# Optimization experiments

Measured on AMD Instinct MI355X. Metric: run time of the kernel, lower is better.

The kernel has to match this reference:

```python
import jax, jax.numpy as jnp
import numpy as np

N = 20000      # nodes
E = 200000     # edges (before self loops)
H = 8          # heads
C = 256        # out_channels per head
IN = 256       # in_channels
OUT = 250      # final linear out


def setup_inputs() -> dict:
    key = jax.random.key(0)
    ks = jax.random.split(key, 8)
    x = jax.random.normal(ks[0], (N, IN), jnp.float32)
    edge_index = jax.random.randint(ks[1], (2, E), 0, N)
    # GATConv params (lin has no bias in PyG; bias is on the conv output)
    W_gat = jax.random.normal(ks[2], (IN, H * C), jnp.float32) * 0.02
    att_src = jax.random.normal(ks[3], (H, C), jnp.float32) * 0.1
    att_dst = jax.random.normal(ks[4], (H, C), jnp.float32) * 0.1
    b_gat = jnp.zeros((H * C,), jnp.float32)
    # conv1: 1x1 conv with 1 in/out channel -> scalar weight + scalar bias
    conv_w = jax.random.normal(ks[5], (), jnp.float32)
    conv_b = jnp.zeros((), jnp.float32)
    W_lin = jax.random.normal(ks[6], (C, OUT), jnp.float32) * 0.02
    b_lin = jnp.zeros((OUT,), jnp.float32)
    return dict(x=x, edge_index=edge_index, W_gat=W_gat, att_src=att_src,
                att_dst=att_dst, b_gat=b_gat, conv_w=conv_w, conv_b=conv_b,
                W_lin=W_lin, b_lin=b_lin)


def reference(x, edge_index, W_gat, att_src, att_dst, b_gat, conv_w, conv_b, W_lin, b_lin):
    # --- GATConv (PyG defaults: add_self_loops=True, negative_slope=0.2, concat=True) ---
    loops = jnp.arange(N)
    src = jnp.concatenate([edge_index[0], loops])  # [E+N]
    dst = jnp.concatenate([edge_index[1], loops])
    xh = (x @ W_gat).reshape(N, H, C)              # [N,H,C]
    a_s = jnp.einsum('nhc,hc->nh', xh, att_src)    # [N,H]
    a_d = jnp.einsum('nhc,hc->nh', xh, att_dst)
    e = jax.nn.leaky_relu(a_s[src] + a_d[dst], 0.2)  # [E+N, H]
    # segment softmax over edges sharing a destination node
    m = jax.ops.segment_max(e, dst, num_segments=N)
    m = jnp.where(jnp.isfinite(m), m, 0.0)
    ex = jnp.exp(e - m[dst])
    s = jax.ops.segment_sum(ex, dst, num_segments=N)
    alpha = ex / (s[dst] + 1e-16)                  # [E+N, H]
    msg = xh[src] * alpha[:, :, None]              # [E+N, H, C]  (dominant traffic)
    agg = jax.ops.segment_sum(msg, dst, num_segments=N)  # [N,H,C]
    agg = agg + b_gat.reshape(H, C)
    # --- head split / pool / 1x1 conv / head softmax / fuse ---
    z = agg.transpose(1, 0, 2)                     # [H,N,C]  (torch z is [H,1,N,C])
    pooled = z.mean(axis=(1, 2))                   # [H] global avg pool
    g = jax.nn.relu(pooled * conv_w + conv_b)
    w = jax.nn.softmax(g, axis=0)                  # softmax over heads (dim=0)
    fuse = jnp.einsum('hnc,h->nc', z, w)           # sum over heads of z * w
    Hf = jax.nn.relu(fuse + x)                     # residual with input features
    return Hf @ W_lin + b_lin                      # [N, 250]
```

## Files before the change

### kernel.cpp

```cpp
#include <hip/hip_runtime.h>
#include <hip/hip_bf16.h>


typedef __attribute__((ext_vector_type(8))) short short8v;
typedef __attribute__((ext_vector_type(4))) float float4v;

__device__ __forceinline__ unsigned f2bfu(float f) {
  unsigned u = __float_as_uint(f);
  return (u + 0x7fffu + ((u >> 16) & 1u)) >> 16;
}
__device__ __forceinline__ float bfu_lo(unsigned u) { return __uint_as_float(u << 16); }
__device__ __forceinline__ float bfu_hi(unsigned u) { return __uint_as_float(u & 0xffff0000u); }
__device__ __forceinline__ unsigned pack2(float a, float b) { return f2bfu(a) | (f2bfu(b) << 16); }

__device__ __forceinline__ void ld8(const float* p, float* v) {
  float4 a = ((const float4*)p)[0], b = ((const float4*)p)[1];
  v[0] = a.x; v[1] = a.y; v[2] = a.z; v[3] = a.w;
  v[4] = b.x; v[5] = b.y; v[6] = b.z; v[7] = b.w;
}
__device__ __forceinline__ void ld4(const float* p, float* v) {
  float4 a = ((const float4*)p)[0];
  v[0] = a.x; v[1] = a.y; v[2] = a.z; v[3] = a.w;
}

__device__ __forceinline__ float bcast(float x, int e) {
  return __uint_as_float((unsigned)__builtin_amdgcn_readlane((int)__float_as_uint(x), e));
}

__device__ __forceinline__ void gll16(const void* g, void* l) {
  __builtin_amdgcn_global_load_lds(
      (__attribute__((address_space(1))) void*)const_cast<void*>(g),
      (__attribute__((address_space(3))) void*)(l), 16, 0, 0);
}

__global__ __launch_bounds__(256) void prep1_kernel(
    const float* __restrict__ W_lin, short* __restrict__ wlT,
    const float* __restrict__ W, const float* __restrict__ att_s,
    const float* __restrict__ att_d, float* __restrict__ ws_s,
    float* __restrict__ ws_d, float* __restrict__ ws_r,
    const int* __restrict__ ei, int* __restrict__ deg) {
  __shared__ float smem[4096];
  int b = blockIdx.x;
  int t = threadIdx.x;
  if (b < 64) {
    float (*tile)[33] = (float(*)[33])smem;
    int tx = t & 31, ty = t >> 5;
    int c0 = (b & 7) * 32, r0 = (b >> 3) * 32;
    #pragma unroll
    for (int j = ty; j < 32; j += 8) {
      int r = r0 + j, c = c0 + tx;
      tile[j][tx] = (c < 250) ? W_lin[(size_t)r * 250 + c] : 0.f;
    }
    __syncthreads();
    #pragma unroll
    for (int j = ty; j < 32; j += 8) {
      int c = c0 + j, r = r0 + tx;
      wlT[(size_t)c * 256 + r] = (short)f2bfu(tile[tx][j]);
    }
  } else if (b < 96) {
    float* sas = smem;
    float* sad = smem + 2048;
    for (int i = t; i < 2048; i += 256) { sas[i] = att_s[i]; sad[i] = att_d[i]; }
    __syncthreads();
    int kk = t >> 5, h = (t >> 2) & 7, q = t & 3;
    int k = (b - 64) * 8 + kk;
    const float4* wr = (const float4*)(W + (size_t)k * 2048 + h * 256 + q * 64);
    const float* as = sas + h * 256 + q * 64;
    const float* ad = sad + h * 256 + q * 64;
    float s = 0.f, dd = 0.f, r = 0.f;
    #pragma unroll
    for (int c4 = 0; c4 < 16; ++c4) {
      float4 wv = wr[c4];
      int c = c4 * 4;
      s  += wv.x * as[c] + wv.y * as[c + 1] + wv.z * as[c + 2] + wv.w * as[c + 3];
      dd += wv.x * ad[c] + wv.y * ad[c + 1] + wv.z * ad[c + 2] + wv.w * ad[c + 3];
      r  += wv.x + wv.y + wv.z + wv.w;
    }
    #pragma unroll
    for (int off = 1; off < 4; off <<= 1) {
      s += __shfl_xor(s, off);
      dd += __shfl_xor(dd, off);
      r += __shfl_xor(r, off);
    }
    if (q == 0) {
      int g = k * 8 + h;
      ws_s[g] = s;
      ws_d[g] = dd;
      ws_r[g] = r;
    }
  } else {
    int e = (b - 96) * 256 + t;
    if (e < 200000) atomicAdd(&deg[ei[200000 + e]], 1);
  }
}

__global__ __launch_bounds__(256) void asd_kernel(const float* __restrict__ x,
    const float* __restrict__ ws_s, const float* __restrict__ ws_d,
    const float* __restrict__ ws_r, float* __restrict__ a_s,
    float* __restrict__ a_d, float* __restrict__ rs, short* __restrict__ x_bf) {
  __shared__ float ls[2048], ld2[2048], lr[2048];
  int tid = threadIdx.x;
  for (int i = tid; i < 2048; i += 256) { ls[i] = ws_s[i]; ld2[i] = ws_d[i]; lr[i] = ws_r[i]; }
  __syncthreads();
  int node = blockIdx.x * 32 + (tid >> 3);
  int h = tid & 7;
  const float4* xr = (const float4*)(x + (size_t)node * 256);
  float as = 0.f, ad = 0.f, rr = 0.f;
  #pragma unroll 1
  for (int g = 0; g < 8; ++g) {
    bool own = (g == h);
    int bufi[16];
    #pragma unroll
    for (int j = 0; j < 8; ++j) {
      int k4 = g * 8 + j;
      float4 v = xr[k4];
      int k8 = k4 * 32 + h;
      as += v.x * ls[k8] + v.y * ls[k8 + 8] + v.z * ls[k8 + 16] + v.w * ls[k8 + 24];
      ad += v.x * ld2[k8] + v.y * ld2[k8 + 8] + v.z * ld2[k8 + 16] + v.w * ld2[k8 + 24];
      rr += v.x * lr[k8] + v.y * lr[k8 + 8] + v.z * lr[k8 + 16] + v.w * lr[k8 + 24];
      bufi[2 * j] = (int)pack2(v.x, v.y);
      bufi[2 * j + 1] = (int)pack2(v.z, v.w);
    }
    if (own) {
      int4* dst = (int4*)(x_bf + (size_t)node * 256 + h * 32);
      dst[0] = make_int4(bufi[0], bufi[1], bufi[2], bufi[3]);
      dst[1] = make_int4(bufi[4], bufi[5], bufi[6], bufi[7]);
      dst[2] = make_int4(bufi[8], bufi[9], bufi[10], bufi[11]);
      dst[3] = make_int4(bufi[12], bufi[13], bufi[14], bufi[15]);
    }
  }
  a_s[node * 8 + h] = as;
  a_d[node * 8 + h] = ad;
  rs[node * 8 + h] = rr;
}

template <int EPI>
__global__ __launch_bounds__(256, 2) void gemm_kernel(
    const short* __restrict__ A, const short* __restrict__ BT,
    int M, int K,
    short* __restrict__ Cb, float* __restrict__ Cf,
    const float* __restrict__ bias, const float* __restrict__ xres, int Nout) {
  __shared__ short lA[64 * 128];
  __shared__ short lB[256 * 128];
  int tid = threadIdx.x;
  int wave = tid >> 6, lane = tid & 63;
  int m0 = blockIdx.x << 6;
  int lr = lane & 15, lq = lane >> 4;
  int lrow4 = lane >> 4;
  int pch = lane & 15;

  float4v acc[4][4];
  #pragma unroll
  for (int i = 0; i < 4; ++i)
    #pragma unroll
    for (int j = 0; j < 4; ++j) acc[i][j] = (float4v){0.f, 0.f, 0.f, 0.f};

  int offA[4];
  #pragma unroll
  for (int it = 0; it < 4; ++it) {
    int rowl = wave * 16 + it * 4 + lrow4;
    int grow = m0 + rowl;
    if (grow >= M) grow = M - 1;
    int logical = pch ^ (rowl & 7);
    offA[it] = grow * K + logical * 8;
  }
  int offB[16];
  #pragma unroll
  for (int it = 0; it < 16; ++it) {
    int rowb = wave * 64 + it * 4 + lrow4;
    int logical = pch ^ (rowb & 7);
    offB[it] = rowb * K + logical * 8;
  }

  int nk = K >> 7;
  for (int t = 0; t < nk; ++t) {
    int k0 = t << 7;
    __syncthreads();
    #pragma unroll
    for (int it = 0; it < 4; ++it)
      gll16(A + offA[it] + k0, lA + (wave * 16 + it * 4) * 128);
    #pragma unroll
    for (int it = 0; it < 16; ++it)
      gll16(BT + offB[it] + k0, lB + (wave * 64 + it * 4) * 128);
    __syncthreads();
    #pragma unroll
    for (int ks = 0; ks < 4; ++ks) {
      int phys = ((ks * 4 + lq) ^ (lr & 7)) * 8;
      short8v af[4], bfv[4];
      #pragma unroll
      for (int i = 0; i < 4; ++i)
        af[i] = *(const short8v*)(lA + (i * 16 + lr) * 128 + phys);
      #pragma unroll
      for (int j = 0; j < 4; ++j)
        bfv[j] = *(const short8v*)(lB + (wave * 64 + j * 16 + lr) * 128 + phys);
      #pragma unroll
      for (int i = 0; i < 4; ++i)
        #pragma unroll
        for (int j = 0; j < 4; ++j)
          acc[i][j] = __builtin_amdgcn_mfma_f32_16x16x32_bf16(af[i], bfv[j], acc[i][j], 0, 0, 0);
    }
  }

  #pragma unroll
  for (int i = 0; i < 4; ++i) {
    #pragma unroll
    for (int jj = 0; jj < 4; ++jj) {
      int row = m0 + i * 16 + lq * 4 + jj;
      if (row >= M) continue;
      #pragma unroll
      for (int j = 0; j < 4; ++j) {
        int col = wave * 64 + j * 16 + lr;
        float v = acc[i][j][jj];
        if (EPI == 1) {
          if (col < Nout) Cf[(size_t)row * Nout + col] = v + bias[col];
        } else {
          float o = v + bias[col] + xres[(size_t)row * 256 + col];
          Cb[(size_t)row * 256 + col] = (short)f2bfu(fmaxf(o, 0.f));
        }
      }
    }
  }
}


__global__ __launch_bounds__(1024) void scan_kernel(const int* __restrict__ deg,
                                                    int* __restrict__ rowptr,
                                                    int* __restrict__ cursor, int n) {
  __shared__ int part[1024];
  int t = threadIdx.x;
  int base = t * 20;
  int loc[20];
  int run = 0;
  #pragma unroll
  for (int j = 0; j < 20; ++j) {
    int idx = base + j;
    int v = (idx < n) ? deg[idx] : 0;
    loc[j] = run;
    run += v;
  }
  part[t] = run;
  __syncthreads();
  for (int off = 1; off < 1024; off <<= 1) {
    int add = (t >= off) ? part[t - off] : 0;
    __syncthreads();
    part[t] += add;
    __syncthreads();
  }
  int off0 = (t > 0) ? part[t - 1] : 0;
  #pragma unroll
  for (int j = 0; j < 20; ++j) {
    int idx = base + j;
    if (idx < n) {
      int v = off0 + loc[j];
      rowptr[idx] = v;
      cursor[idx] = v;
    }
  }
  if (t == 1023) rowptr[n] = part[1023];
}

__global__ void scatter_kernel(const int* __restrict__ ei, int* __restrict__ cursor,
                               int* __restrict__ csr_src, int E) {
  int e = blockIdx.x * 256 + threadIdx.x;
  if (e < E) {
    int pos = atomicAdd(&cursor[ei[E + e]], 1);
    csr_src[pos] = ei[e];
  }
}

__global__ __launch_bounds__(256) void alphaz_kernel(
    const short* __restrict__ x_bf, const float* __restrict__ a_s,
    const float* __restrict__ a_d, const float* __restrict__ rs,
    const int* __restrict__ rowptr, const int* __restrict__ csr,
    short* __restrict__ u, float* __restrict__ pp) {
  int gw = blockIdx.x * 4 + (threadIdx.x >> 6);
  int d = gw >> 1;
  int wh = (gw & 1) * 4;
  int lane = threadIdx.x & 63;
  int beg = rowptr[d];
  int deg = rowptr[d + 1] - beg;

  float ad[4];
  ld4(a_d + (size_t)d * 8 + wh, ad);

  float acc[4][4];
  #pragma unroll
  for (int h = 0; h < 4; ++h)
    #pragma unroll
    for (int j = 0; j < 4; ++j) acc[h][j] = 0.f;
  float s4[4], p4[4];

  {
    float t[4], rsv[4];
    ld4(a_s + (size_t)d * 8 + wh, t);
    ld4(rs + (size_t)d * 8 + wh, rsv);
    uint2 v = *(const uint2*)(x_bf + (size_t)d * 256 + lane * 4);
    float xv0 = bfu_lo(v.x), xv1 = bfu_hi(v.x), xv2 = bfu_lo(v.y), xv3 = bfu_hi(v.y);
    float lz = (lane == 0) ? 1.f : 0.f;
    #pragma unroll
    for (int h = 0; h < 4; ++h) {
      float e = t[h] + ad[h];
      e = (e > 0.f) ? e : 0.2f * e;
      float ex = __expf(e);
      acc[h][0] += ex * xv0;
      acc[h][1] += ex * xv1;
      acc[h][2] += ex * xv2;
      acc[h][3] += ex * xv3;
      s4[h] = ex * lz;
      p4[h] = ex * rsv[h] * lz;
    }
  }

  for (int base = 0; base < deg; base += 64) {
    int i = base + lane;
    bool act = i < deg;
    int src = act ? csr[beg + i] : 0;
    float ex[4];
    {
      float t[4], rsv[4];
      ld4(a_s + (size_t)src * 8 + wh, t);
      ld4(rs + (size_t)src * 8 + wh, rsv);
      #pragma unroll
      for (int h = 0; h < 4; ++h) {
        float e = t[h] + ad[h];
        e = (e > 0.f) ? e : 0.2f * e;
        float xx = __expf(e);
        ex[h] = act ? xx : 0.f;
        s4[h] += ex[h];
        p4[h] += ex[h] * rsv[h];
      }
    }
    int cnt = deg - base;
    if (cnt > 64) cnt = 64;
    int e = 0;
    for (; e + 1 < cnt; e += 2) {
      int s0 = __builtin_amdgcn_readlane(src, e);
      int s1 = __builtin_amdgcn_readlane(src, e + 1);
      uint2 v0 = *(const uint2*)(x_bf + (size_t)s0 * 256 + lane * 4);
      uint2 v1 = *(const uint2*)(x_bf + (size_t)s1 * 256 + lane * 4);
      float q0[4], q1[4];
      #pragma unroll
      for (int h = 0; h < 4; ++h) { q0[h] = bcast(ex[h], e); q1[h] = bcast(ex[h], e + 1); }
      float a0 = bfu_lo(v0.x), a1 = bfu_hi(v0.x), a2 = bfu_lo(v0.y), a3 = bfu_hi(v0.y);
      float b0 = bfu_lo(v1.x), b1 = bfu_hi(v1.x), b2 = bfu_lo(v1.y), b3 = bfu_hi(v1.y);
      #pragma unroll
      for (int h = 0; h < 4; ++h) {
        acc[h][0] += q0[h] * a0 + q1[h] * b0;
        acc[h][1] += q0[h] * a1 + q1[h] * b1;
        acc[h][2] += q0[h] * a2 + q1[h] * b2;
        acc[h][3] += q0[h] * a3 + q1[h] * b3;
      }
    }
    if (e < cnt) {
      int s0 = __builtin_amdgcn_readlane(src, e);
      uint2 v0 = *(const uint2*)(x_bf + (size_t)s0 * 256 + lane * 4);
      float q0[4];
      #pragma unroll
      for (int h = 0; h < 4; ++h) q0[h] = bcast(ex[h], e);
      float a0 = bfu_lo(v0.x), a1 = bfu_hi(v0.x), a2 = bfu_lo(v0.y), a3 = bfu_hi(v0.y);
      #pragma unroll
      for (int h = 0; h < 4; ++h) {
        acc[h][0] += q0[h] * a0;
        acc[h][1] += q0[h] * a1;
        acc[h][2] += q0[h] * a2;
        acc[h][3] += q0[h] * a3;
      }
    }
  }

  #pragma unroll
  for (int off = 1; off < 64; off <<= 1)
    #pragma unroll
    for (int h = 0; h < 4; ++h) {
      s4[h] += __shfl_xor(s4[h], off);
      p4[h] += __shfl_xor(p4[h], off);
    }
  float inv[4];
  #pragma unroll
  for (int h = 0; h < 4; ++h) inv[h] = 1.f / (s4[h] + 1e-16f);
  #pragma unroll
  for (int h = 0; h < 4; ++h) {
    uint2 ov;
    ov.x = pack2(acc[h][0] * inv[h], acc[h][1] * inv[h]);
    ov.y = pack2(acc[h][2] * inv[h], acc[h][3] * inv[h]);
    *(uint2*)(u + (size_t)d * 2048 + (wh + h) * 256 + lane * 4) = ov;
  }
  if (lane == 0) {
    float4 pn;
    pn.x = p4[0] * inv[0];
    pn.y = p4[1] * inv[1];
    pn.z = p4[2] * inv[2];
    pn.w = p4[3] * inv[3];
    *(float4*)(pp + (size_t)d * 8 + wh) = pn;
  }
}

__global__ __launch_bounds__(256) void reduce_pp_kernel(const float* __restrict__ pp,
                                                        float* __restrict__ pooled) {
  int tid = threadIdx.x;
  float loc[8] = {0, 0, 0, 0, 0, 0, 0, 0};
  for (int r = blockIdx.x * 256 + tid; r < 20000; r += 80 * 256) {
    float t[8];
    ld8(pp + (size_t)r * 8, t);
    #pragma unroll
    for (int h = 0; h < 8; ++h) loc[h] += t[h];
  }
  #pragma unroll
  for (int off = 1; off < 64; off <<= 1)
    #pragma unroll
    for (int h = 0; h < 8; ++h) loc[h] += __shfl_xor(loc[h], off);
  __shared__ float sred[4][8];
  int wave = tid >> 6, lane = tid & 63;
  if (lane == 0) {
    #pragma unroll
    for (int h = 0; h < 8; ++h) sred[wave][h] = loc[h];
  }
  __syncthreads();
  if (tid < 8) {
    atomicAdd(&pooled[tid], sred[0][tid] + sred[1][tid] + sred[2][tid] + sred[3][tid]);
  }
}

__global__ __launch_bounds__(256) void headwfb_kernel(const float* __restrict__ pooled,
    const float* __restrict__ b_gat, const float* __restrict__ conv_w,
    const float* __restrict__ conv_b, float* __restrict__ wsoft,
    float* __restrict__ fb) {
  __shared__ float sb[8];
  __shared__ float sw[8];
  int t = threadIdx.x;
  float v = 0.f;
  #pragma unroll
  for (int j = 0; j < 8; ++j) v += b_gat[t * 8 + j];
  #pragma unroll
  for (int off = 1; off < 32; off <<= 1) v += __shfl_xor(v, off);
  if ((t & 31) == 0) sb[t >> 5] = v;
  __syncthreads();
  if (t == 0) {
    const float invNC = 1.0f / (20000.0f * 256.0f);
    float g[8];
    float mx = -1e30f;
    #pragma unroll
    for (int h = 0; h < 8; ++h) {
      float pm = (pooled[h] + 20000.0f * sb[h]) * invNC;
      float gv = pm * conv_w[0] + conv_b[0];
      gv = fmaxf(gv, 0.f);
      g[h] = gv;
      mx = fmaxf(mx, gv);
    }
    float ssum = 0.f;
    #pragma unroll
    for (int h = 0; h < 8; ++h) { g[h] = __expf(g[h] - mx); ssum += g[h]; }
    #pragma unroll
    for (int h = 0; h < 8; ++h) {
      float w = g[h] / ssum;
      wsoft[h] = w;
      sw[h] = w;
    }
  }
  __syncthreads();
  float a = 0.f;
  #pragma unroll
  for (int h = 0; h < 8; ++h) a += sw[h] * b_gat[h * 256 + t];
  fb[t] = a;
}

__global__ void wmix_kernel(const float* __restrict__ W, const float* __restrict__ wsoft,
                            short* __restrict__ out) {
  __shared__ float tile[32][33];
  int tx = threadIdx.x, ty = threadIdx.y;
  int h = blockIdx.z;
  float wh = wsoft[h];
  int c0 = blockIdx.x * 32, k0 = blockIdx.y * 32;
  #pragma unroll
  for (int j = ty; j < 32; j += 8)
    tile[j][tx] = W[(size_t)(k0 + j) * 2048 + h * 256 + c0 + tx];
  __syncthreads();
  #pragma unroll
  for (int j = ty; j < 32; j += 8)
    out[(size_t)(c0 + j) * 2048 + h * 256 + k0 + tx] = (short)f2bfu(wh * tile[tx][j]);
}

extern "C" void kernel_launch(void* const* d_in, const int* in_sizes, int n_in,
                              void* d_out, int out_size, void* d_ws, size_t ws_size,
                              hipStream_t stream) {
  (void)in_sizes; (void)n_in; (void)out_size; (void)ws_size;
  const float* x      = (const float*)d_in[0];
  const int*   ei     = (const int*)d_in[1];
  const float* W_gat  = (const float*)d_in[2];
  const float* att_s  = (const float*)d_in[3];
  const float* att_d  = (const float*)d_in[4];
  const float* b_gat  = (const float*)d_in[5];
  const float* conv_w = (const float*)d_in[6];
  const float* conv_b = (const float*)d_in[7];
  const float* W_lin  = (const float*)d_in[8];
  const float* b_lin  = (const float*)d_in[9];
  float* out = (float*)d_out;

  char* p = (char*)d_ws;
  size_t off = 0;
  auto alloc = [&](size_t bytes) -> void* {
    void* r = p + off;
    off = (off + bytes + 255) & ~(size_t)255;
    return r;
  };
  short* x_bf   = (short*)alloc((size_t)20000 * 256 * 2);
  short* wmixT  = (short*)alloc((size_t)256 * 2048 * 2);
  short* wlT    = (short*)alloc((size_t)256 * 256 * 2);
  float* ws_s   = (float*)alloc(2048 * 4);
  float* ws_d   = (float*)alloc(2048 * 4);
  float* ws_r   = (float*)alloc(2048 * 4);
  float* a_s    = (float*)alloc((size_t)20000 * 8 * 4);
  float* a_d    = (float*)alloc((size_t)20000 * 8 * 4);
  float* rs     = (float*)alloc((size_t)20000 * 8 * 4);
  int*   deg    = (int*)alloc(20000 * 4);
  float* pooled = (float*)alloc(8 * 4);
  float* wsoft  = (float*)alloc(8 * 4);
  float* fb     = (float*)alloc(256 * 4);
  int*   rowptr = (int*)alloc(20001 * 4);
  int*   cursor = (int*)alloc(20000 * 4);
  int*   csr    = (int*)alloc(200000 * 4);
  float* pp     = (float*)alloc((size_t)20000 * 8 * 4);
  short* u      = (short*)alloc((size_t)20000 * 2048 * 2);
  short* Hf     = x_bf;

  hipMemsetAsync(deg, 0, 20000 * 4, stream);
  hipMemsetAsync(pooled, 0, 8 * 4, stream);

  prep1_kernel<<<878, 256, 0, stream>>>(W_lin, wlT, W_gat, att_s, att_d,
                                        ws_s, ws_d, ws_r, ei, deg);
  scan_kernel<<<1, 1024, 0, stream>>>(deg, rowptr, cursor, 20000);
  asd_kernel<<<625, 256, 0, stream>>>(x, ws_s, ws_d, ws_r, a_s, a_d, rs, x_bf);
  scatter_kernel<<<782, 256, 0, stream>>>(ei, cursor, csr, 200000);
  alphaz_kernel<<<10000, 256, 0, stream>>>(x_bf, a_s, a_d, rs, rowptr, csr, u, pp);
  reduce_pp_kernel<<<80, 256, 0, stream>>>(pp, pooled);
  headwfb_kernel<<<1, 256, 0, stream>>>(pooled, b_gat, conv_w, conv_b, wsoft, fb);
  wmix_kernel<<<dim3(8, 8, 8), dim3(32, 8), 0, stream>>>(W_gat, wsoft, wmixT);
  gemm_kernel<2><<<313, 256, 0, stream>>>(u, wmixT, 20000, 2048,
                                          Hf, nullptr, fb, x, 256);
  gemm_kernel<1><<<313, 256, 0, stream>>>(Hf, wlT, 20000, 256,
                                          nullptr, out, b_lin, nullptr, 250);
}
```

Before: 200.6 us.

## Fuse final two GEMMs and process all heads per wave in aggregation

Merges the mixing GEMM and the output linear GEMM into one kernel, which reuses the block's Hf tile right after writing it and saves a launch. Rewrites the aggregation kernel so each wave covers all eight heads for one destination node, with the two half-waves taking alternate edges. This halves redundant source-row gathers and edge-weight loads. In exchange it uses more registers (a 64-float accumulator) and reads global Hf within the block without an explicit memory fence.

After: 208.2 us. +3.8%, slower.

```diff
diff --git a/kernel.cpp b/kernel.cpp
--- a/kernel.cpp
+++ b/kernel.cpp
@@ -17,10 +17,6 @@
   float4 a = ((const float4*)p)[0], b = ((const float4*)p)[1];
   v[0] = a.x; v[1] = a.y; v[2] = a.z; v[3] = a.w;
   v[4] = b.x; v[5] = b.y; v[6] = b.z; v[7] = b.w;
-}
-__device__ __forceinline__ void ld4(const float* p, float* v) {
-  float4 a = ((const float4*)p)[0];
-  v[0] = a.x; v[1] = a.y; v[2] = a.z; v[3] = a.w;
 }
 
 __device__ __forceinline__ float bcast(float x, int e) {
@@ -134,12 +130,11 @@
   rs[node * 8 + h] = rr;
 }
 
-template <int EPI>
-__global__ __launch_bounds__(256, 2) void gemm_kernel(
-    const short* __restrict__ A, const short* __restrict__ BT,
-    int M, int K,
-    short* __restrict__ Cb, float* __restrict__ Cf,
-    const float* __restrict__ bias, const float* __restrict__ xres, int Nout) {
+__global__ __launch_bounds__(256, 2) void gemm_fused_kernel(
+    const short* __restrict__ u, const short* __restrict__ wmixT,
+    const short* __restrict__ wlT, short* __restrict__ Hf,
+    float* __restrict__ out, const float* __restrict__ fb,
+    const float* __restrict__ x, const float* __restrict__ b_lin, int M) {
   __shared__ short lA[64 * 128];
   __shared__ short lB[256 * 128];
   int tid = threadIdx.x;
@@ -155,33 +150,31 @@
     #pragma unroll
     for (int j = 0; j < 4; ++j) acc[i][j] = (float4v){0.f, 0.f, 0.f, 0.f};
 
-  int offA[4];
+  int rowlA[4], growA[4], logA[4];
   #pragma unroll
   for (int it = 0; it < 4; ++it) {
-    int rowl = wave * 16 + it * 4 + lrow4;
-    int grow = m0 + rowl;
+    rowlA[it] = wave * 16 + it * 4 + lrow4;
+    int grow = m0 + rowlA[it];
     if (grow >= M) grow = M - 1;
-    int logical = pch ^ (rowl & 7);
-    offA[it] = grow * K + logical * 8;
-  }
-  int offB[16];
+    growA[it] = grow;
+    logA[it] = pch ^ (rowlA[it] & 7);
+  }
+  int rowB[16], logB[16];
   #pragma unroll
   for (int it = 0; it < 16; ++it) {
-    int rowb = wave * 64 + it * 4 + lrow4;
-    int logical = pch ^ (rowb & 7);
-    offB[it] = rowb * K + logical * 8;
-  }
-
-  int nk = K >> 7;
-  for (int t = 0; t < nk; ++t) {
+    rowB[it] = wave * 64 + it * 4 + lrow4;
+    logB[it] = pch ^ (rowB[it] & 7);
+  }
+
+  for (int t = 0; t < 16; ++t) {
     int k0 = t << 7;
     __syncthreads();
     #pragma unroll
     for (int it = 0; it < 4; ++it)
-      gll16(A + offA[it] + k0, lA + (wave * 16 + it * 4) * 128);
+      gll16(u + (size_t)growA[it] * 2048 + logA[it] * 8 + k0, lA + (wave * 16 + it * 4) * 128);
     #pragma unroll
     for (int it = 0; it < 16; ++it)
-      gll16(BT + offB[it] + k0, lB + (wave * 64 + it * 4) * 128);
+      gll16(wmixT + (size_t)rowB[it] * 2048 + logB[it] * 8 + k0, lB + (wave * 64 + it * 4) * 128);
     __syncthreads();
     #pragma unroll
     for (int ks = 0; ks < 4; ++ks) {
@@ -200,7 +193,6 @@
           acc[i][j] = __builtin_amdgcn_mfma_f32_16x16x32_bf16(af[i], bfv[j], acc[i][j], 0, 0, 0);
     }
   }
-
   #pragma unroll
   for (int i = 0; i < 4; ++i) {
     #pragma unroll
@@ -210,13 +202,54 @@
       #pragma unroll
       for (int j = 0; j < 4; ++j) {
         int col = wave * 64 + j * 16 + lr;
-        float v = acc[i][j][jj];
-        if (EPI == 1) {
-          if (col < Nout) Cf[(size_t)row * Nout + col] = v + bias[col];
-        } else {
-          float o = v + bias[col] + xres[(size_t)row * 256 + col];
-          Cb[(size_t)row * 256 + col] = (short)f2bfu(fmaxf(o, 0.f));
-        }
+        float o = acc[i][j][jj] + fb[col] + x[(size_t)row * 256 + col];
+        Hf[(size_t)row * 256 + col] = (short)f2bfu(fmaxf(o, 0.f));
+      }
+    }
+  }
+
+  #pragma unroll
+  for (int i = 0; i < 4; ++i)
+    #pragma unroll
+    for (int j = 0; j < 4; ++j) acc[i][j] = (float4v){0.f, 0.f, 0.f, 0.f};
+
+  for (int t = 0; t < 2; ++t) {
+    int k0 = t << 7;
+    __syncthreads();
+    #pragma unroll
+    for (int it = 0; it < 4; ++it)
+      gll16(Hf + (size_t)growA[it] * 256 + logA[it] * 8 + k0, lA + (wave * 16 + it * 4) * 128);
+    #pragma unroll
+    for (int it = 0; it < 16; ++it)
+      gll16(wlT + (size_t)rowB[it] * 256 + logB[it] * 8 + k0, lB + (wave * 64 + it * 4) * 128);
+    __syncthreads();
+    #pragma unroll
+    for (int ks = 0; ks < 4; ++ks) {
+      int phys = ((ks * 4 + lq) ^ (lr & 7)) * 8;
+      short8v af[4], bfv[4];
+      #pragma unroll
+      for (int i = 0; i < 4; ++i)
+        af[i] = *(const short8v*)(lA + (i * 16 + lr) * 128 + phys);
+      #pragma unroll
+      for (int j = 0; j < 4; ++j)
+        bfv[j] = *(const short8v*)(lB + (wave * 64 + j * 16 + lr) * 128 + phys);
+      #pragma unroll
+      for (int i = 0; i < 4; ++i)
+        #pragma unroll
+        for (int j = 0; j < 4; ++j)
+          acc[i][j] = __builtin_amdgcn_mfma_f32_16x16x32_bf16(af[i], bfv[j], acc[i][j], 0, 0, 0);
+    }
+  }
+  #pragma unroll
+  for (int i = 0; i < 4; ++i) {
+    #pragma unroll
+    for (int jj = 0; jj < 4; ++jj) {
+      int row = m0 + i * 16 + lq * 4 + jj;
+      if (row >= M) continue;
+      #pragma unroll
+      for (int j = 0; j < 4; ++j) {
+        int col = wave * 64 + j * 16 + lr;
+        if (col < 250) out[(size_t)row * 250 + col] = acc[i][j][jj] + b_lin[col];
       }
     }
   }
@@ -273,125 +306,119 @@
     const float* __restrict__ a_d, const float* __restrict__ rs,
     const int* __restrict__ rowptr, const int* __restrict__ csr,
     short* __restrict__ u, float* __restrict__ pp) {
-  int gw = blockIdx.x * 4 + (threadIdx.x >> 6);
-  int d = gw >> 1;
-  int wh = (gw & 1) * 4;
+  int d = blockIdx.x * 4 + (threadIdx.x >> 6);
   int lane = threadIdx.x & 63;
+  int half = lane >> 5;
+  int cl = (lane & 31) * 8;
   int beg = rowptr[d];
   int deg = rowptr[d + 1] - beg;
-
-  float ad[4];
-  ld4(a_d + (size_t)d * 8 + wh, ad);
-
-  float acc[4][4];
-  #pragma unroll
-  for (int h = 0; h < 4; ++h)
-    #pragma unroll
-    for (int j = 0; j < 4; ++j) acc[h][j] = 0.f;
-  float s4[4], p4[4];
-
-  {
-    float t[4], rsv[4];
-    ld4(a_s + (size_t)d * 8 + wh, t);
-    ld4(rs + (size_t)d * 8 + wh, rsv);
-    uint2 v = *(const uint2*)(x_bf + (size_t)d * 256 + lane * 4);
-    float xv0 = bfu_lo(v.x), xv1 = bfu_hi(v.x), xv2 = bfu_lo(v.y), xv3 = bfu_hi(v.y);
-    float lz = (lane == 0) ? 1.f : 0.f;
-    #pragma unroll
-    for (int h = 0; h < 4; ++h) {
-      float e = t[h] + ad[h];
-      e = (e > 0.f) ? e : 0.2f * e;
-      float ex = __expf(e);
-      acc[h][0] += ex * xv0;
-      acc[h][1] += ex * xv1;
-      acc[h][2] += ex * xv2;
-      acc[h][3] += ex * xv3;
-      s4[h] = ex * lz;
-      p4[h] = ex * rsv[h] * lz;
-    }
-  }
-
-  for (int base = 0; base < deg; base += 64) {
+  int nb = deg + 1;
+
+  float ad8[8];
+  ld8(a_d + (size_t)d * 8, ad8);
+
+  float acc[8][8];
+  #pragma unroll
+  for (int h = 0; h < 8; ++h)
+    #pragma unroll
+    for (int c = 0; c < 8; ++c) acc[h][c] = 0.f;
+  float s8[8] = {0, 0, 0, 0, 0, 0, 0, 0};
+  float p8[8] = {0, 0, 0, 0, 0, 0, 0, 0};
+
+  for (int base = 0; base < nb; base += 64) {
     int i = base + lane;
-    bool act = i < deg;
-    int src = act ? csr[beg + i] : 0;
-    float ex[4];
+    bool act = i < nb;
+    int srcv = d;
+    if (i < deg) srcv = csr[beg + i];
+    float ex[8];
     {
-      float t[4], rsv[4];
-      ld4(a_s + (size_t)src * 8 + wh, t);
-      ld4(rs + (size_t)src * 8 + wh, rsv);
-      #pragma unroll
-      for (int h = 0; h < 4; ++h) {
-        float e = t[h] + ad[h];
+      float t8[8], r8[8];
+      ld8(a_s + (size_t)srcv * 8, t8);
+      ld8(rs + (size_t)srcv * 8, r8);
+      #pragma unroll
+      for (int h = 0; h < 8; ++h) {
+        float e = t8[h] + ad8[h];
         e = (e > 0.f) ? e : 0.2f * e;
-        float xx = __expf(e);
-        ex[h] = act ? xx : 0.f;
-        s4[h] += ex[h];
-        p4[h] += ex[h] * rsv[h];
+        float xx = act ? __expf(e) : 0.f;
+        ex[h] = xx;
+        s8[h] += xx;
+        p8[h] += xx * r8[h];
       }
     }
-    int cnt = deg - base;
+    int cnt = nb - base;
     if (cnt > 64) cnt = 64;
     int e = 0;
     for (; e + 1 < cnt; e += 2) {
-      int s0 = __builtin_amdgcn_readlane(src, e);
-      int s1 = __builtin_amdgcn_readlane(src, e + 1);
-      uint2 v0 = *(const uint2*)(x_bf + (size_t)s0 * 256 + lane * 4);
-      uint2 v1 = *(const uint2*)(x_bf + (size_t)s1 * 256 + lane * 4);
-      float q0[4], q1[4];
-      #pragma unroll
-      for (int h = 0; h < 4; ++h) { q0[h] = bcast(ex[h], e); q1[h] = bcast(ex[h], e + 1); }
-      float a0 = bfu_lo(v0.x), a1 = bfu_hi(v0.x), a2 = bfu_lo(v0.y), a3 = bfu_hi(v0.y);
-      float b0 = bfu_lo(v1.x), b1 = bfu_hi(v1.x), b2 = bfu_lo(v1.y), b3 = bfu_hi(v1.y);
-      #pragma unroll
-      for (int h = 0; h < 4; ++h) {
-        acc[h][0] += q0[h] * a0 + q1[h] * b0;
-        acc[h][1] += q0[h] * a1 + q1[h] * b1;
-        acc[h][2] += q0[h] * a2 + q1[h] * b2;
-        acc[h][3] += q0[h] * a3 + q1[h] * b3;
+      int s0 = __builtin_amdgcn_readlane(srcv, e);
+      int s1 = __builtin_amdgcn_readlane(srcv, e + 1);
+      int ss = half ? s1 : s0;
+      uint4 v = *(const uint4*)(x_bf + (size_t)ss * 256 + cl);
+      float q[8];
+      #pragma unroll
+      for (int h = 0; h < 8; ++h) {
+        float qa = bcast(ex[h], e), qb = bcast(ex[h], e + 1);
+        q[h] = half ? qb : qa;
       }
+      float xv[8];
+      xv[0] = bfu_lo(v.x); xv[1] = bfu_hi(v.x);
+      xv[2] = bfu_lo(v.y); xv[3] = bfu_hi(v.y);
+      xv[4] = bfu_lo(v.z); xv[5] = bfu_hi(v.z);
+      xv[6] = bfu_lo(v.w); xv[7] = bfu_hi(v.w);
+      #pragma unroll
+      for (int h = 0; h < 8; ++h)
+        #pragma unroll
+        for (int c = 0; c < 8; ++c) acc[h][c] += q[h] * xv[c];
     }
     if (e < cnt) {
-      int s0 = __builtin_amdgcn_readlane(src, e);
-      uint2 v0 = *(const uint2*)(x_bf + (size_t)s0 * 256 + lane * 4);
-      float q0[4];
-      #pragma unroll
-      for (int h = 0; h < 4; ++h) q0[h] = bcast(ex[h], e);
-      float a0 = bfu_lo(v0.x), a1 = bfu_hi(v0.x), a2 = bfu_lo(v0.y), a3 = bfu_hi(v0.y);
-      #pragma unroll
-      for (int h = 0; h < 4; ++h) {
-        acc[h][0] += q0[h] * a0;
-        acc[h][1] += q0[h] * a1;
-        acc[h][2] += q0[h] * a2;
-        acc[h][3] += q0[h] * a3;
-      }
-    }
-  }
-
+      int s0 = __builtin_amdgcn_readlane(srcv, e);
+      uint4 v = *(const uint4*)(x_bf + (size_t)s0 * 256 + cl);
+      float q[8];
+      #pragma unroll
+      for (int h = 0; h < 8; ++h) q[h] = half ? 0.f : bcast(ex[h], e);
+      float xv[8];
+      xv[0] = bfu_lo(v.x); xv[1] = bfu_hi(v.x);
+      xv[2] = bfu_lo(v.y); xv[3] = bfu_hi(v.y);
+      xv[4] = bfu_lo(v.z); xv[5] = bfu_hi(v.z);
+      xv[6] = bfu_lo(v.w); xv[7] = bfu_hi(v.w);
+      #pragma unroll
+      for (int h = 0; h < 8; ++h)
+        #pragma unroll
+        for (int c = 0; c < 8; ++c) acc[h][c] += q[h] * xv[c];
+    }
+  }
+
+  #pragma unroll
+  for (int h = 0; h < 8; ++h)
+    #pragma unroll
+    for (int c = 0; c < 8; ++c) acc[h][c] += __shfl_xor(acc[h][c], 32);
   #pragma unroll
   for (int off = 1; off < 64; off <<= 1)
     #pragma unroll
-    for (int h = 0; h < 4; ++h) {
-      s4[h] += __shfl_xor(s4[h], off);
-      p4[h] += __shfl_xor(p4[h], off);
-    }
-  float inv[4];
-  #pragma unroll
-  for (int h = 0; h < 4; ++h) inv[h] = 1.f / (s4[h] + 1e-16f);
-  #pragma unroll
-  for (int h = 0; h < 4; ++h) {
-    uint2 ov;
-    ov.x = pack2(acc[h][0] * inv[h], acc[h][1] * inv[h]);
-    ov.y = pack2(acc[h][2] * inv[h], acc[h][3] * inv[h]);
-    *(uint2*)(u + (size_t)d * 2048 + (wh + h) * 256 + lane * 4) = ov;
+    for (int h = 0; h < 8; ++h) {
+      s8[h] += __shfl_xor(s8[h], off);
+      p8[h] += __shfl_xor(p8[h], off);
+    }
+  float inv[8];
+  #pragma unroll
+  for (int h = 0; h < 8; ++h) inv[h] = 1.f / (s8[h] + 1e-16f);
+
+  if (half == 0) {
+    #pragma unroll
+    for (int h = 0; h < 8; ++h) {
+      uint4 ov;
+      ov.x = pack2(acc[h][0] * inv[h], acc[h][1] * inv[h]);
+      ov.y = pack2(acc[h][2] * inv[h], acc[h][3] * inv[h]);
+      ov.z = pack2(acc[h][4] * inv[h], acc[h][5] * inv[h]);
+      ov.w = pack2(acc[h][6] * inv[h], acc[h][7] * inv[h]);
+      *(uint4*)(u + (size_t)d * 2048 + h * 256 + cl) = ov;
+    }
   }
   if (lane == 0) {
-    float4 pn;
-    pn.x = p4[0] * inv[0];
-    pn.y = p4[1] * inv[1];
-    pn.z = p4[2] * inv[2];
-    pn.w = p4[3] * inv[3];
-    *(float4*)(pp + (size_t)d * 8 + wh) = pn;
+    float pn[8];
+    #pragma unroll
+    for (int h = 0; h < 8; ++h) pn[h] = p8[h] * inv[h];
+    ((float4*)(pp + (size_t)d * 8))[0] = make_float4(pn[0], pn[1], pn[2], pn[3]);
+    ((float4*)(pp + (size_t)d * 8))[1] = make_float4(pn[4], pn[5], pn[6], pn[7]);
   }
 }
 
@@ -531,12 +558,9 @@
   scan_kernel<<<1, 1024, 0, stream>>>(deg, rowptr, cursor, 20000);
   asd_kernel<<<625, 256, 0, stream>>>(x, ws_s, ws_d, ws_r, a_s, a_d, rs, x_bf);
   scatter_kernel<<<782, 256, 0, stream>>>(ei, cursor, csr, 200000);
-  alphaz_kernel<<<10000, 256, 0, stream>>>(x_bf, a_s, a_d, rs, rowptr, csr, u, pp);
+  alphaz_kernel<<<5000, 256, 0, stream>>>(x_bf, a_s, a_d, rs, rowptr, csr, u, pp);
   reduce_pp_kernel<<<80, 256, 0, stream>>>(pp, pooled);
   headwfb_kernel<<<1, 256, 0, stream>>>(pooled, b_gat, conv_w, conv_b, wsoft, fb);
   wmix_kernel<<<dim3(8, 8, 8), dim3(32, 8), 0, stream>>>(W_gat, wsoft, wmixT);
-  gemm_kernel<2><<<313, 256, 0, stream>>>(u, wmixT, 20000, 2048,
-                                          Hf, nullptr, fb, x, 256);
-  gemm_kernel<1><<<313, 256, 0, stream>>>(Hf, wlT, 20000, 256,
-                                          nullptr, out, b_lin, nullptr, 250);
-}
+  gemm_fused_kernel<<<313, 256, 0, stream>>>(u, wmixT, wlT, Hf, out, fb, x, b_lin, 20000);
+}
```
